# Optimization experiments

Hardware: AMD Instinct MI355X
Metric: run time of the kernel (lower is better)

Reference implementation:

```python
import jax, jax.numpy as jnp
import numpy as np

N = 100000
E = 1600000
IN_C = 128
OUT_C = 128


def setup_inputs() -> dict:
    key = jax.random.key(0)
    k1, k2, k3, k4, k5, k6 = jax.random.split(key, 6)
    x = jax.random.normal(k1, (N, IN_C), dtype=jnp.float32)
    edge_row = jax.random.randint(k2, (E,), 0, N, dtype=jnp.int32)  # dst nodes
    edge_col = jax.random.randint(k3, (E,), 0, N, dtype=jnp.int32)  # src nodes
    scale = 1.0 / np.sqrt(IN_C)
    W_l = jax.random.normal(k4, (IN_C, OUT_C), dtype=jnp.float32) * scale
    b_l = jax.random.normal(k5, (OUT_C,), dtype=jnp.float32) * 0.01
    W_r = jax.random.normal(k6, (IN_C, OUT_C), dtype=jnp.float32) * scale
    return {"x": x, "edge_row": edge_row, "edge_col": edge_col,
            "W_l": W_l, "b_l": b_l, "W_r": W_r}


def reference(x, edge_row, edge_col, W_l, b_l, W_r):
    # SAGEConv with mean aggregation over adj_t (edge_row=dst, edge_col=src)
    msgs = x[edge_col]                                   # [E, IN_C] gather
    summed = jax.ops.segment_sum(msgs, edge_row, num_segments=N)  # [N, IN_C]
    deg = jax.ops.segment_sum(jnp.ones((E,), dtype=x.dtype), edge_row,
                              num_segments=N)            # [N]
    agg = summed / jnp.maximum(deg, 1.0)[:, None]        # mean aggregation
    out = agg @ W_l + b_l + x @ W_r                      # lin_l(agg) + lin_r(x_dst)
    return jax.nn.relu(out)
```

## Files before the change

kernel.cpp:

```cpp
#include <hip/hip_runtime.h>

#define N_NODES 100000
#define E_EDGES 1600000
#define C 128
#define BSHIFT 9
#define BMASK 511
#define BNODES 512
#define NBKT 196

#define PA2_BLOCKS 196
#define CAP2 80
#define RUNSTRIDE (PA2_BLOCKS * CAP2)

#define PB_BLOCKS 196
#define CVT_BLOCKS 1563
#define PACK_BLOCKS 4

typedef __attribute__((ext_vector_type(8))) short short8;
typedef __attribute__((ext_vector_type(4))) float f32x4;

__device__ __forceinline__ unsigned short f2bf(float f) {
  unsigned int b = __float_as_uint(f);
  return (unsigned short)((b + 0x7fffu + ((b >> 16) & 1u)) >> 16);
}
__device__ __forceinline__ float bflo(unsigned int v) {
  return __uint_as_float(v << 16);
}
__device__ __forceinline__ float bfhi(unsigned int v) {
  return __uint_as_float(v & 0xffff0000u);
}

__global__ __launch_bounds__(512) void passA_kernel(
    const int* __restrict__ erow, const int* __restrict__ ecol,
    int* __restrict__ pairs, int* __restrict__ cntmat) {
  __shared__ int cnt[NBKT];
  int bid = blockIdx.x;
  int tid = threadIdx.x;

  for (int b = tid; b < NBKT; b += 512) cnt[b] = 0;
  __syncthreads();

#pragma unroll
  for (int k = 0; k < 4; ++k) {
    int idx = bid * 2048 + k * 512 + tid;
    if (idx < E_EDGES / 4) {
      int4 r = ((const int4*)erow)[idx];
      int4 c = ((const int4*)ecol)[idx];
      int d[4] = {r.x, r.y, r.z, r.w};
      int s[4] = {c.x, c.y, c.z, c.w};
#pragma unroll
      for (int i = 0; i < 4; ++i) {
        int bk = d[i] >> BSHIFT;
        int rk = atomicAdd(&cnt[bk], 1);
        if (rk < CAP2)
          pairs[(bk * PA2_BLOCKS + bid) * CAP2 + rk] =
              (s[i] << BSHIFT) | (d[i] & BMASK);
      }
    }
  }
  __syncthreads();
  for (int b = tid; b < NBKT; b += 512) cntmat[bid * NBKT + b] = cnt[b];
}

__global__ __launch_bounds__(1024) void passB_kernel(
    const int* __restrict__ pairs, const int* __restrict__ cntmat,
    const float* __restrict__ x, const float* __restrict__ W_l,
    const float* __restrict__ W_r, ushort* __restrict__ xh,
    ushort* __restrict__ Bp, int* __restrict__ deg, int* __restrict__ ssrc,
    int capn) {
  int bid = blockIdx.x;
  int t = threadIdx.x;

  if (bid < PB_BLOCKS) {
    __shared__ int l[BNODES];
    __shared__ int llen[PA2_BLOCKS];
    int b = bid;
    if (t < BNODES) l[t] = 0;
    if (t < PA2_BLOCKS) llen[t] = min(cntmat[t * NBKT + b], CAP2);
    __syncthreads();

    int nbase = b << BSHIFT;
    int nn = min(BNODES, N_NODES - nbase);
    const int* bp = pairs + b * RUNSTRIDE;
    int wbase = nbase * capn;

    for (int e = t; e < RUNSTRIDE; e += 1024) {
      int run = e / CAP2;
      int off = e - run * CAP2;
      if (off < llen[run]) {
        int p = bp[e];
        int loc = p & BMASK;
        int slot = atomicAdd(&l[loc], 1);
        if (slot < capn) ssrc[wbase + loc * capn + slot] = p >> BSHIFT;
      }
    }
    __syncthreads();
    if (t < nn) deg[nbase + t] = l[t];
  } else if (bid < PB_BLOCKS + CVT_BLOCKS) {
    int t2 = (bid - PB_BLOCKS) * 1024 + t;
    if (t2 < (N_NODES * C) / 8) {
      float4 a = ((const float4*)x)[2 * t2];
      float4 b = ((const float4*)x)[2 * t2 + 1];
      ushort u[8] = {f2bf(a.x), f2bf(a.y), f2bf(a.z), f2bf(a.w),
                     f2bf(b.x), f2bf(b.y), f2bf(b.z), f2bf(b.w)};
      ((uint4*)xh)[t2] = *(const uint4*)u;
    }
  } else {
    int tt = (bid - PB_BLOCKS - CVT_BLOCKS) * 1024 + t;
    int Cb = tt >> 9, kb = (tt >> 6) & 7, lane = tt & 63;
    int n = Cb * 16 + (lane & 15);
    int k0 = kb * 32 + (lane >> 4) * 8;
    ushort u[8];
#pragma unroll
    for (int j = 0; j < 8; ++j) {
      int k = k0 + j;
      float w = (k < C) ? W_l[k * C + n] : W_r[(k - C) * C + n];
      u[j] = f2bf(w);
    }
    ((uint4*)Bp)[tt] = *(const uint4*)u;
  }
}

__global__ __launch_bounds__(256) void fused_kernel(
    const ushort* __restrict__ xh, const int* __restrict__ deg,
    const int* __restrict__ ssrc, const ushort* __restrict__ Bp,
    const float* __restrict__ b_l, float* __restrict__ out, int capn) {
  __shared__ ushort lA[32][264];
  int tid = threadIdx.x;
  int lane = tid & 63;
  int wave = tid >> 6;
  long base = (long)blockIdx.x * 32;

  for (int i = tid; i < 32 * 16; i += 256) {
    int r = i >> 4, q = i & 15;
    uint4 v = ((const uint4*)(xh + (base + r) * C))[q];
    *(uint4*)&lA[r][128 + q * 8] = v;
  }

  int l4 = lane & 15;
  int q = lane >> 4;

  for (int j = 0; j < 8; ++j) {
    int n = wave * 8 + j;
    int row = (int)base + n;
    int dg = deg[row];
    int e0 = row * capn;
    int e1 = e0 + min(dg, capn);
    float s[8];
#pragma unroll
    for (int i = 0; i < 8; ++i) s[i] = 0.0f;

    int e = e0 + q;
    for (; e + 4 < e1; e += 8) {
      int sa = ssrc[e];
      int sb = ssrc[e + 4];
      uint4 va = ((const uint4*)(xh + (long)sa * C))[l4];
      uint4 vb = ((const uint4*)(xh + (long)sb * C))[l4];
      s[0] += bflo(va.x) + bflo(vb.x); s[1] += bfhi(va.x) + bfhi(vb.x);
      s[2] += bflo(va.y) + bflo(vb.y); s[3] += bfhi(va.y) + bfhi(vb.y);
      s[4] += bflo(va.z) + bflo(vb.z); s[5] += bfhi(va.z) + bfhi(vb.z);
      s[6] += bflo(va.w) + bflo(vb.w); s[7] += bfhi(va.w) + bfhi(vb.w);
    }
    if (e < e1) {
      int sa = ssrc[e];
      uint4 va = ((const uint4*)(xh + (long)sa * C))[l4];
      s[0] += bflo(va.x); s[1] += bfhi(va.x);
      s[2] += bflo(va.y); s[3] += bfhi(va.y);
      s[4] += bflo(va.z); s[5] += bfhi(va.z);
      s[6] += bflo(va.w); s[7] += bfhi(va.w);
    }
#pragma unroll
    for (int i = 0; i < 8; ++i) {
      s[i] += __shfl_xor(s[i], 16);
      s[i] += __shfl_xor(s[i], 32);
    }
    float inv = 1.0f / fmaxf((float)dg, 1.0f);
    if (q == 0) {
      ushort u[8];
#pragma unroll
      for (int i = 0; i < 8; ++i) u[i] = f2bf(s[i] * inv);
      *(uint4*)&lA[n][l4 * 8] = *(const uint4*)u;
    }
  }
  __syncthreads();

  f32x4 acc0 = {0, 0, 0, 0}, acc1 = {0, 0, 0, 0};
  f32x4 acc2 = {0, 0, 0, 0}, acc3 = {0, 0, 0, 0};
  int m = lane & 15, quad = lane >> 4;
  const ushort* bp0 = Bp + (((2 * wave + 0) * 8) * 64 + lane) * 8;
  const ushort* bp1 = Bp + (((2 * wave + 1) * 8) * 64 + lane) * 8;
#pragma unroll
  for (int kb = 0; kb < 8; ++kb) {
    short8 a0 = *(const short8*)&lA[m][kb * 32 + quad * 8];
    short8 a1 = *(const short8*)&lA[16 + m][kb * 32 + quad * 8];
    short8 b0 = *(const short8*)(bp0 + kb * 64 * 8);
    short8 b1 = *(const short8*)(bp1 + kb * 64 * 8);
    acc0 = __builtin_amdgcn_mfma_f32_16x16x32_bf16(a0, b0, acc0, 0, 0, 0);
    acc1 = __builtin_amdgcn_mfma_f32_16x16x32_bf16(a0, b1, acc1, 0, 0, 0);
    acc2 = __builtin_amdgcn_mfma_f32_16x16x32_bf16(a1, b0, acc2, 0, 0, 0);
    acc3 = __builtin_amdgcn_mfma_f32_16x16x32_bf16(a1, b1, acc3, 0, 0, 0);
  }

  int col0 = (2 * wave + 0) * 16 + m;
  int col1 = col0 + 16;
  float bl0 = b_l[col0], bl1 = b_l[col1];
#pragma unroll
  for (int r = 0; r < 4; ++r) {
    long row0 = base + quad * 4 + r;
    long row1 = row0 + 16;
    out[row0 * C + col0] = fmaxf(acc0[r] + bl0, 0.0f);
    out[row0 * C + col1] = fmaxf(acc1[r] + bl1, 0.0f);
    out[row1 * C + col0] = fmaxf(acc2[r] + bl0, 0.0f);
    out[row1 * C + col1] = fmaxf(acc3[r] + bl1, 0.0f);
  }
}

extern "C" void kernel_launch(void* const* d_in, const int* in_sizes, int n_in,
                              void* d_out, int out_size, void* d_ws, size_t ws_size,
                              hipStream_t stream) {
  const float* x   = (const float*)d_in[0];
  const int* erow  = (const int*)d_in[1];
  const int* ecol  = (const int*)d_in[2];
  const float* W_l = (const float*)d_in[3];
  const float* b_l = (const float*)d_in[4];
  const float* W_r = (const float*)d_in[5];
  float* out = (float*)d_out;

  char* p = (char*)d_ws;
  ushort* xh  = (ushort*)p;  p += (size_t)N_NODES * C * 2;
  ushort* Bp  = (ushort*)p;  p += 2 * C * C * 2;
  int* deg    = (int*)p;     p += (size_t)N_NODES * 4;
  int* cntmat = (int*)p;     p += (size_t)PA2_BLOCKS * NBKT * 4;
  int* pairs  = (int*)p;     p += (size_t)NBKT * RUNSTRIDE * 4;
  int* ssrc   = (int*)p;

  size_t base_used = (size_t)(p - (char*)d_ws);
  int capn = 40;
  if (ws_size >= base_used + (size_t)N_NODES * 64 * 4) capn = 64;
  else if (ws_size >= base_used + (size_t)N_NODES * 48 * 4) capn = 48;

  passA_kernel<<<PA2_BLOCKS, 512, 0, stream>>>(erow, ecol, pairs, cntmat);
  passB_kernel<<<PB_BLOCKS + CVT_BLOCKS + PACK_BLOCKS, 1024, 0, stream>>>(
      pairs, cntmat, x, W_l, W_r, xh, Bp, deg, ssrc, capn);
  fused_kernel<<<N_NODES / 32, 256, 0, stream>>>(xh, deg, ssrc, Bp, b_l, out, capn);
}
```

Before: 216.3 us.

## Build compact per-bucket CSR with prefix-scan offsets instead of fixed-capacity slots

After: 205.6 us. 1.05x faster.

```diff
diff --git a/kernel.cpp b/kernel.cpp
--- a/kernel.cpp
+++ b/kernel.cpp
@@ -8,13 +8,14 @@
 #define BNODES 512
 #define NBKT 196
 
-#define PA2_BLOCKS 196
+#define PA_BLOCKS 196
 #define CAP2 80
-#define RUNSTRIDE (PA2_BLOCKS * CAP2)
+#define RUNSTRIDE (PA_BLOCKS * CAP2)
+#define PACK_BLOCKS 8
 
 #define PB_BLOCKS 196
 #define CVT_BLOCKS 1563
-#define PACK_BLOCKS 4
+#define BCAP 8704
 
 typedef __attribute__((ext_vector_type(8))) short short8;
 typedef __attribute__((ext_vector_type(4))) float f32x4;
@@ -32,71 +33,112 @@
 
 __global__ __launch_bounds__(512) void passA_kernel(
     const int* __restrict__ erow, const int* __restrict__ ecol,
-    int* __restrict__ pairs, int* __restrict__ cntmat) {
+    const float* __restrict__ W_l, const float* __restrict__ W_r,
+    ushort* __restrict__ Bp, int* __restrict__ pairs,
+    int* __restrict__ cntmat) {
   __shared__ int cnt[NBKT];
   int bid = blockIdx.x;
   int tid = threadIdx.x;
 
-  for (int b = tid; b < NBKT; b += 512) cnt[b] = 0;
-  __syncthreads();
-
-#pragma unroll
-  for (int k = 0; k < 4; ++k) {
-    int idx = bid * 2048 + k * 512 + tid;
-    if (idx < E_EDGES / 4) {
-      int4 r = ((const int4*)erow)[idx];
-      int4 c = ((const int4*)ecol)[idx];
-      int d[4] = {r.x, r.y, r.z, r.w};
-      int s[4] = {c.x, c.y, c.z, c.w};
-#pragma unroll
-      for (int i = 0; i < 4; ++i) {
-        int bk = d[i] >> BSHIFT;
-        int rk = atomicAdd(&cnt[bk], 1);
-        if (rk < CAP2)
-          pairs[(bk * PA2_BLOCKS + bid) * CAP2 + rk] =
-              (s[i] << BSHIFT) | (d[i] & BMASK);
-      }
-    }
-  }
-  __syncthreads();
-  for (int b = tid; b < NBKT; b += 512) cntmat[bid * NBKT + b] = cnt[b];
+  if (bid < PA_BLOCKS) {
+    for (int b = tid; b < NBKT; b += 512) cnt[b] = 0;
+    __syncthreads();
+
+#pragma unroll
+    for (int k = 0; k < 4; ++k) {
+      int idx = bid * 2048 + k * 512 + tid;
+      if (idx < E_EDGES / 4) {
+        int4 r = ((const int4*)erow)[idx];
+        int4 c = ((const int4*)ecol)[idx];
+        int d[4] = {r.x, r.y, r.z, r.w};
+        int s[4] = {c.x, c.y, c.z, c.w};
+#pragma unroll
+        for (int i = 0; i < 4; ++i) {
+          int bk = d[i] >> BSHIFT;
+          int rk = atomicAdd(&cnt[bk], 1);
+          if (rk < CAP2)
+            pairs[(bk * PA_BLOCKS + bid) * CAP2 + rk] =
+                (s[i] << BSHIFT) | (d[i] & BMASK);
+        }
+      }
+    }
+    __syncthreads();
+    for (int b = tid; b < NBKT; b += 512) cntmat[bid * NBKT + b] = cnt[b];
+  } else {
+    int t = (bid - PA_BLOCKS) * 512 + tid;
+    int Cb = t >> 9, kb = (t >> 6) & 7, lane = t & 63;
+    int n = Cb * 16 + (lane & 15);
+    int k0 = kb * 32 + (lane >> 4) * 8;
+    ushort u[8];
+#pragma unroll
+    for (int j = 0; j < 8; ++j) {
+      int k = k0 + j;
+      float w = (k < C) ? W_l[k * C + n] : W_r[(k - C) * C + n];
+      u[j] = f2bf(w);
+    }
+    ((uint4*)Bp)[t] = *(const uint4*)u;
+  }
 }
 
 __global__ __launch_bounds__(1024) void passB_kernel(
     const int* __restrict__ pairs, const int* __restrict__ cntmat,
-    const float* __restrict__ x, const float* __restrict__ W_l,
-    const float* __restrict__ W_r, ushort* __restrict__ xh,
-    ushort* __restrict__ Bp, int* __restrict__ deg, int* __restrict__ ssrc,
-    int capn) {
+    const float* __restrict__ x, ushort* __restrict__ xh,
+    int* __restrict__ deg, int* __restrict__ offv, int* __restrict__ ssrc) {
   int bid = blockIdx.x;
   int t = threadIdx.x;
 
   if (bid < PB_BLOCKS) {
     __shared__ int l[BNODES];
-    __shared__ int llen[PA2_BLOCKS];
+    __shared__ int cur[BNODES];
+    __shared__ int llen[PA_BLOCKS];
     int b = bid;
     if (t < BNODES) l[t] = 0;
-    if (t < PA2_BLOCKS) llen[t] = min(cntmat[t * NBKT + b], CAP2);
-    __syncthreads();
-
-    int nbase = b << BSHIFT;
-    int nn = min(BNODES, N_NODES - nbase);
+    for (int r = t; r < PA_BLOCKS; r += 1024)
+      llen[r] = min(cntmat[r * NBKT + b], CAP2);
+    __syncthreads();
+
     const int* bp = pairs + b * RUNSTRIDE;
-    int wbase = nbase * capn;
-
     for (int e = t; e < RUNSTRIDE; e += 1024) {
       int run = e / CAP2;
       int off = e - run * CAP2;
       if (off < llen[run]) {
         int p = bp[e];
-        int loc = p & BMASK;
-        int slot = atomicAdd(&l[loc], 1);
-        if (slot < capn) ssrc[wbase + loc * capn + slot] = p >> BSHIFT;
-      }
-    }
-    __syncthreads();
-    if (t < nn) deg[nbase + t] = l[t];
-  } else if (bid < PB_BLOCKS + CVT_BLOCKS) {
+        atomicAdd(&l[p & BMASK], 1);
+      }
+    }
+    __syncthreads();
+
+    int own = (t < BNODES) ? l[t] : 0;
+    for (int d = 1; d < BNODES; d <<= 1) {
+      int u = (t < BNODES && t >= d) ? l[t - d] : 0;
+      __syncthreads();
+      if (t < BNODES) l[t] += u;
+      __syncthreads();
+    }
+    if (t < BNODES) {
+      int excl = l[t] - own;
+      int nbase = b << BSHIFT;
+      int node = nbase + t;
+      int ex = min(excl, BCAP);
+      int dg = min(own, BCAP - ex);
+      if (node < N_NODES) {
+        offv[node] = b * BCAP + ex;
+        deg[node] = dg;
+      }
+      cur[t] = excl;
+    }
+    __syncthreads();
+
+    for (int e = t; e < RUNSTRIDE; e += 1024) {
+      int run = e / CAP2;
+      int off = e - run * CAP2;
+      if (off < llen[run]) {
+        int p = bp[e];
+        int s = atomicAdd(&cur[p & BMASK], 1);
+        if (s < BCAP) ssrc[b * BCAP + s] = p >> BSHIFT;
+      }
+    }
+  } else {
     int t2 = (bid - PB_BLOCKS) * 1024 + t;
     if (t2 < (N_NODES * C) / 8) {
       float4 a = ((const float4*)x)[2 * t2];
@@ -105,26 +147,14 @@
                      f2bf(b.x), f2bf(b.y), f2bf(b.z), f2bf(b.w)};
       ((uint4*)xh)[t2] = *(const uint4*)u;
     }
-  } else {
-    int tt = (bid - PB_BLOCKS - CVT_BLOCKS) * 1024 + t;
-    int Cb = tt >> 9, kb = (tt >> 6) & 7, lane = tt & 63;
-    int n = Cb * 16 + (lane & 15);
-    int k0 = kb * 32 + (lane >> 4) * 8;
-    ushort u[8];
-#pragma unroll
-    for (int j = 0; j < 8; ++j) {
-      int k = k0 + j;
-      float w = (k < C) ? W_l[k * C + n] : W_r[(k - C) * C + n];
-      u[j] = f2bf(w);
-    }
-    ((uint4*)Bp)[tt] = *(const uint4*)u;
   }
 }
 
 __global__ __launch_bounds__(256) void fused_kernel(
     const ushort* __restrict__ xh, const int* __restrict__ deg,
-    const int* __restrict__ ssrc, const ushort* __restrict__ Bp,
-    const float* __restrict__ b_l, float* __restrict__ out, int capn) {
+    const int* __restrict__ offv, const int* __restrict__ ssrc,
+    const ushort* __restrict__ Bp, const float* __restrict__ b_l,
+    float* __restrict__ out) {
   __shared__ ushort lA[32][264];
   int tid = threadIdx.x;
   int lane = tid & 63;
@@ -144,8 +174,8 @@
     int n = wave * 8 + j;
     int row = (int)base + n;
     int dg = deg[row];
-    int e0 = row * capn;
-    int e1 = e0 + min(dg, capn);
+    int e0 = offv[row];
+    int e1 = e0 + dg;
     float s[8];
 #pragma unroll
     for (int i = 0; i < 8; ++i) s[i] = 0.0f;
@@ -230,17 +260,15 @@
   ushort* xh  = (ushort*)p;  p += (size_t)N_NODES * C * 2;
   ushort* Bp  = (ushort*)p;  p += 2 * C * C * 2;
   int* deg    = (int*)p;     p += (size_t)N_NODES * 4;
-  int* cntmat = (int*)p;     p += (size_t)PA2_BLOCKS * NBKT * 4;
+  int* offv   = (int*)p;     p += (size_t)N_NODES * 4;
+  int* cntmat = (int*)p;     p += (size_t)PA_BLOCKS * NBKT * 4;
   int* pairs  = (int*)p;     p += (size_t)NBKT * RUNSTRIDE * 4;
   int* ssrc   = (int*)p;
 
-  size_t base_used = (size_t)(p - (char*)d_ws);
-  int capn = 40;
-  if (ws_size >= base_used + (size_t)N_NODES * 64 * 4) capn = 64;
-  else if (ws_size >= base_used + (size_t)N_NODES * 48 * 4) capn = 48;
-
-  passA_kernel<<<PA2_BLOCKS, 512, 0, stream>>>(erow, ecol, pairs, cntmat);
-  passB_kernel<<<PB_BLOCKS + CVT_BLOCKS + PACK_BLOCKS, 1024, 0, stream>>>(
-      pairs, cntmat, x, W_l, W_r, xh, Bp, deg, ssrc, capn);
-  fused_kernel<<<N_NODES / 32, 256, 0, stream>>>(xh, deg, ssrc, Bp, b_l, out, capn);
-}
+  passA_kernel<<<PA_BLOCKS + PACK_BLOCKS, 512, 0, stream>>>(
+      erow, ecol, W_l, W_r, Bp, pairs, cntmat);
+  passB_kernel<<<PB_BLOCKS + CVT_BLOCKS, 1024, 0, stream>>>(
+      pairs, cntmat, x, xh, deg, offv, ssrc);
+  fused_kernel<<<N_NODES / 32, 256, 0, stream>>>(xh, deg, offv, ssrc, Bp, b_l,
+                                                 out);
+}
```
